# Kernel tuning notes

Measured on AMD Instinct MI355X. Metric: run time of the kernel, lower is better.

Reference implementation:

```python
import jax, jax.numpy as jnp
import numpy as np

I, H, O = 8, 32, 1  # input_size, hidden_size, output_size


def setup_inputs() -> dict:
    key = jax.random.key(0)
    ks = jax.random.split(key, 7)
    B, T = 4096, 256
    s_ih = 1.0 / np.sqrt(H)
    inp = {
        "x": jax.random.normal(ks[0], (B, T, I), dtype=jnp.float32),
        # PyTorch nn.LSTM params, gate order [i, f, g, o]
        "W_ih": jax.random.uniform(ks[1], (4 * H, I), minval=-s_ih, maxval=s_ih, dtype=jnp.float32),
        "W_hh": jax.random.uniform(ks[2], (4 * H, H), minval=-s_ih, maxval=s_ih, dtype=jnp.float32),
        "b_ih": jax.random.uniform(ks[3], (4 * H,), minval=-s_ih, maxval=s_ih, dtype=jnp.float32),
        "b_hh": jax.random.uniform(ks[4], (4 * H,), minval=-s_ih, maxval=s_ih, dtype=jnp.float32),
        # nn.Linear(H, O)
        "W_out": jax.random.uniform(ks[5], (O, H), minval=-s_ih, maxval=s_ih, dtype=jnp.float32),
        "b_out": jax.random.uniform(ks[6], (O,), minval=-s_ih, maxval=s_ih, dtype=jnp.float32),
    }
    return inp


def _lstm_last_h(x, W_ih, W_hh, b_ih, b_hh):
    B = x.shape[0]
    # Precompute input projections for all steps: [T, B, 4H]
    x_proj = jnp.einsum("bti,gi->tbg", x, W_ih) + (b_ih + b_hh)
    h0 = jnp.zeros((B, H), dtype=x.dtype)
    c0 = jnp.zeros((B, H), dtype=x.dtype)

    def step(carry, xp):
        h, c = carry
        z = xp + h @ W_hh.T  # [B, 4H]
        i = jax.nn.sigmoid(z[:, 0 * H:1 * H])
        f = jax.nn.sigmoid(z[:, 1 * H:2 * H])
        g = jnp.tanh(z[:, 2 * H:3 * H])
        o = jax.nn.sigmoid(z[:, 3 * H:4 * H])
        c = f * c + i * g
        h = o * jnp.tanh(c)
        return (h, c), None

    (hT, _), _ = jax.lax.scan(step, (h0, c0), x_proj)
    return hT  # equals out[:, -1, :] for unidirectional batch_first LSTM


def reference(x, W_ih, W_hh, b_ih, b_hh, W_out, b_out):
    hT = _lstm_last_h(x, W_ih, W_hh, b_ih, b_hh)
    return hT @ W_out.T + b_out  # [B, O]
```

## Files before the change

kernel.cpp:

```cpp
#include <hip/hip_runtime.h>


#define T_LEN   256
#define HALF_T  128
#define XSTRIDE 130
#define LOG2E   1.4426950408889634f

typedef short bf16x8 __attribute__((ext_vector_type(8)));
typedef float f32x4  __attribute__((ext_vector_type(4)));
typedef unsigned u32x4 __attribute__((ext_vector_type(4)));

static __device__ inline short f2bf_rne(float f) {
    union { float f; unsigned u; } v; v.f = f;
    unsigned u = v.u;
    return (short)((u + 0x7FFFu + ((u >> 16) & 1u)) >> 16);
}
static __device__ inline unsigned pack_bf2(float a, float b) {
    union { float f; unsigned u; } x, y; x.f = a; y.f = b;
    return ((x.u + 0x8000u) >> 16) | ((y.u + 0x8000u) & 0xFFFF0000u);
}
static __device__ inline float bf2f(short s) {
    union { unsigned u; float f; } v;
    v.u = ((unsigned)(unsigned short)s) << 16;
    return v.f;
}

__global__ __launch_bounds__(256) void lstm_kernel(
    const float* __restrict__ x, const float* __restrict__ W_ih,
    const float* __restrict__ W_hh, const float* __restrict__ b_ih,
    const float* __restrict__ b_hh, const float* __restrict__ W_out,
    const float* __restrict__ b_out, float* __restrict__ out)
{
    __shared__ __attribute__((aligned(16))) short xl[HALF_T * XSTRIDE];
    __shared__ __attribute__((aligned(16))) short h_lds[2][16 * 40];

    const int tid  = threadIdx.x;
    const int w    = tid >> 6;
    const int lane = tid & 63;
    const int L    = lane & 15;
    const int q    = lane >> 4;
    const int row0 = blockIdx.x * 16;
    const float4* xv = (const float4*)x;

    bf16x8 whh[2], wih[2];
    f32x4  bias[2];
#pragma unroll
    for (int e = 0; e < 2; ++e) {
        const int   n = 32 * (L & 3) + 8 * (L >> 2) + 2 * w + e;
        const float s = ((L & 3) == 2 ? 2.f * LOG2E : LOG2E);
        const float* src = W_hh + n * 32 + q * 8;
        bf16x8 fr;
#pragma unroll
        for (int j = 0; j < 8; ++j) fr[j] = f2bf_rne(src[j] * s);
        whh[e] = fr;
        bf16x8 gr = (bf16x8){0,0,0,0,0,0,0,0};
        if (q == 0) {
            const float* s2 = W_ih + n * 8;
#pragma unroll
            for (int j = 0; j < 8; ++j) gr[j] = f2bf_rne(s2[j] * s);
        }
        wih[e] = gr;
        f32x4 bb;
#pragma unroll
        for (int r = 0; r < 4; ++r) {
            const int   nr = 32 * r + 8 * q + 2 * w + e;
            const float sr = (r == 2 ? 2.f * LOG2E : LOG2E);
            bb[r] = (b_ih[nr] + b_hh[nr]) * sr;
        }
        bias[e] = bb;
    }

    for (int i = tid; i < 16 * 40; i += 256) h_lds[0][i] = 0;

#pragma unroll
    for (int it = 0; it < 8; ++it) {
        const int idx = tid + (it << 8);
        const int L2  = idx >> 7;
        const int tl  = idx & (HALF_T - 1);
        const float4* srcp = xv + ((size_t)(row0 + L2) * T_LEN + tl) * 2;
        const float4 a = srcp[0], b = srcp[1];
        u32x4 u;
        u[0] = pack_bf2(a.x, a.y); u[1] = pack_bf2(a.z, a.w);
        u[2] = pack_bf2(b.x, b.y); u[3] = pack_bf2(b.z, b.w);
        *(u32x4*)(&xl[tl * XSTRIDE + L2 * 8]) = u;
    }
    __syncthreads();

    f32x4 zx[2];
    {
        const bf16x8 xf0 = *(const bf16x8*)(&xl[L * 8]);
        zx[0] = __builtin_amdgcn_mfma_f32_16x16x32_bf16(wih[0], xf0, bias[0], 0, 0, 0);
        zx[1] = __builtin_amdgcn_mfma_f32_16x16x32_bf16(wih[1], xf0, bias[1], 0, 0, 0);
    }

    float c0 = 0.f, c1 = 0.f;

#pragma unroll 2
    for (int t = 0; t < T_LEN; ++t) {
        if (t == HALF_T - 1) {
#pragma unroll
            for (int it = 0; it < 8; ++it) {
                const int idx = tid + (it << 8);
                const int L2  = idx >> 7;
                const int tl  = idx & (HALF_T - 1);
                const float4* srcp = xv + ((size_t)(row0 + L2) * T_LEN + HALF_T + tl) * 2;
                const float4 a = srcp[0], b = srcp[1];
                u32x4 u;
                u[0] = pack_bf2(a.x, a.y); u[1] = pack_bf2(a.z, a.w);
                u[2] = pack_bf2(b.x, b.y); u[3] = pack_bf2(b.z, b.w);
                *(u32x4*)(&xl[tl * XSTRIDE + L2 * 8]) = u;
            }
            __syncthreads();
        }

        const int par = t & 1, nxt = par ^ 1;

        const bf16x8 hfrag = *(const bf16x8*)(&h_lds[par][L * 40 + q * 8]);
        int tn = t + 1; if (tn >= T_LEN) tn = T_LEN - 1;
        const bf16x8 xfrag = *(const bf16x8*)(&xl[(tn & (HALF_T - 1)) * XSTRIDE + L * 8]);

        const f32x4 a0 = __builtin_amdgcn_mfma_f32_16x16x32_bf16(whh[0], hfrag, zx[0], 0, 0, 0);
        const f32x4 a1 = __builtin_amdgcn_mfma_f32_16x16x32_bf16(whh[1], hfrag, zx[1], 0, 0, 0);
        zx[0] = __builtin_amdgcn_mfma_f32_16x16x32_bf16(wih[0], xfrag, bias[0], 0, 0, 0);
        zx[1] = __builtin_amdgcn_mfma_f32_16x16x32_bf16(wih[1], xfrag, bias[1], 0, 0, 0);

        float h0, h1;
        {
            const float ei = __builtin_amdgcn_exp2f(-a0[0]);
            const float ef = __builtin_amdgcn_exp2f(-a0[1]);
            const float eg = __builtin_amdgcn_exp2f(-a0[2]);
            const float eo = __builtin_amdgcn_exp2f(-a0[3]);
            const float fv = __builtin_amdgcn_rcpf(1.f + ef);
            const float ig = (1.f - eg) * __builtin_amdgcn_rcpf((1.f + ei) * (1.f + eg));
            c0 = fmaf(fv, c0, ig);
            const float ec = __builtin_amdgcn_exp2f(fminf(c0 * (-2.f * LOG2E), 40.f));
            h0 = (1.f - ec) * __builtin_amdgcn_rcpf((1.f + eo) * (1.f + ec));
        }
        {
            const float ei = __builtin_amdgcn_exp2f(-a1[0]);
            const float ef = __builtin_amdgcn_exp2f(-a1[1]);
            const float eg = __builtin_amdgcn_exp2f(-a1[2]);
            const float eo = __builtin_amdgcn_exp2f(-a1[3]);
            const float fv = __builtin_amdgcn_rcpf(1.f + ef);
            const float ig = (1.f - eg) * __builtin_amdgcn_rcpf((1.f + ei) * (1.f + eg));
            c1 = fmaf(fv, c1, ig);
            const float ec = __builtin_amdgcn_exp2f(fminf(c1 * (-2.f * LOG2E), 40.f));
            h1 = (1.f - ec) * __builtin_amdgcn_rcpf((1.f + eo) * (1.f + ec));
        }

        *(unsigned*)(&h_lds[nxt][L * 40 + 8 * q + 2 * w]) = pack_bf2(h0, h1);

        __syncthreads();
    }

    if (tid < 16) {
        float s = b_out[0];
#pragma unroll
        for (int k = 0; k < 32; ++k) s = fmaf(bf2f(h_lds[0][tid * 40 + k]), W_out[k], s);
        out[row0 + tid] = s;
    }
}

extern "C" void kernel_launch(void* const* d_in, const int* in_sizes, int n_in,
                              void* d_out, int out_size, void* d_ws, size_t ws_size,
                              hipStream_t stream) {
    const float* x     = (const float*)d_in[0];
    const float* W_ih  = (const float*)d_in[1];
    const float* W_hh  = (const float*)d_in[2];
    const float* b_ih  = (const float*)d_in[3];
    const float* b_hh  = (const float*)d_in[4];
    const float* W_out = (const float*)d_in[5];
    const float* b_out = (const float*)d_in[6];
    float* out = (float*)d_out;

    const int B = in_sizes[0] / (T_LEN * 8);
    const int tiles = B / 16;
    lstm_kernel<<<tiles, 256, 0, stream>>>(x, W_ih, W_hh, b_ih, b_hh, W_out, b_out, out);
}
```

Baseline: 147.8 us.

## Halve batch rows per block to double block count and occupancy

Each block now handles 8 batch rows instead of 16, launching twice as many blocks, with the x staging buffer halved and launch bounds requesting two blocks per CU. The MFMA N dimension still spans 16 columns, so rows are duplicated (L&7) and half the compute is redundant. The weight row mapping is permuted across waves, and the next-step input projection MFMA is moved after the h store to overlap with the barrier. The intent is more parallelism across CUs and latency hiding for the serial recurrence, at the cost of wasted MFMA work.

```diff
diff --git a/kernel.cpp b/kernel.cpp
--- a/kernel.cpp
+++ b/kernel.cpp
@@ -3,7 +3,7 @@
 
 #define T_LEN   256
 #define HALF_T  128
-#define XSTRIDE 130
+#define XSTRIDE 66
 #define LOG2E   1.4426950408889634f
 
 typedef short bf16x8 __attribute__((ext_vector_type(8)));
@@ -25,7 +25,7 @@
     return v.f;
 }
 
-__global__ __launch_bounds__(256) void lstm_kernel(
+__global__ __launch_bounds__(256, 2) void lstm_kernel(
     const float* __restrict__ x, const float* __restrict__ W_ih,
     const float* __restrict__ W_hh, const float* __restrict__ b_ih,
     const float* __restrict__ b_hh, const float* __restrict__ W_out,
@@ -39,31 +39,31 @@
     const int lane = tid & 63;
     const int L    = lane & 15;
     const int q    = lane >> 4;
-    const int row0 = blockIdx.x * 16;
+    const int rbase = blockIdx.x * 8;
     const float4* xv = (const float4*)x;
 
     bf16x8 whh[2], wih[2];
     f32x4  bias[2];
 #pragma unroll
     for (int e = 0; e < 2; ++e) {
-        const int   n = 32 * (L & 3) + 8 * (L >> 2) + 2 * w + e;
-        const float s = ((L & 3) == 2 ? 2.f * LOG2E : LOG2E);
+        const int   n  = 32 * (L & 3) + 8 * w + 2 * (L >> 2) + e;
+        const float sc = ((L & 3) == 2 ? 2.f * LOG2E : LOG2E);
         const float* src = W_hh + n * 32 + q * 8;
         bf16x8 fr;
 #pragma unroll
-        for (int j = 0; j < 8; ++j) fr[j] = f2bf_rne(src[j] * s);
+        for (int j = 0; j < 8; ++j) fr[j] = f2bf_rne(src[j] * sc);
         whh[e] = fr;
         bf16x8 gr = (bf16x8){0,0,0,0,0,0,0,0};
         if (q == 0) {
             const float* s2 = W_ih + n * 8;
 #pragma unroll
-            for (int j = 0; j < 8; ++j) gr[j] = f2bf_rne(s2[j] * s);
+            for (int j = 0; j < 8; ++j) gr[j] = f2bf_rne(s2[j] * sc);
         }
         wih[e] = gr;
         f32x4 bb;
 #pragma unroll
         for (int r = 0; r < 4; ++r) {
-            const int   nr = 32 * r + 8 * q + 2 * w + e;
+            const int   nr = 32 * r + 8 * w + 2 * q + e;
             const float sr = (r == 2 ? 2.f * LOG2E : LOG2E);
             bb[r] = (b_ih[nr] + b_hh[nr]) * sr;
         }
@@ -73,11 +73,11 @@
     for (int i = tid; i < 16 * 40; i += 256) h_lds[0][i] = 0;
 
 #pragma unroll
-    for (int it = 0; it < 8; ++it) {
+    for (int it = 0; it < 4; ++it) {
         const int idx = tid + (it << 8);
+        const int tl  = idx & (HALF_T - 1);
         const int L2  = idx >> 7;
-        const int tl  = idx & (HALF_T - 1);
-        const float4* srcp = xv + ((size_t)(row0 + L2) * T_LEN + tl) * 2;
+        const float4* srcp = xv + ((size_t)(rbase + L2) * T_LEN + tl) * 2;
         const float4 a = srcp[0], b = srcp[1];
         u32x4 u;
         u[0] = pack_bf2(a.x, a.y); u[1] = pack_bf2(a.z, a.w);
@@ -88,22 +88,23 @@
 
     f32x4 zx[2];
     {
-        const bf16x8 xf0 = *(const bf16x8*)(&xl[L * 8]);
+        const bf16x8 xf0 = *(const bf16x8*)(&xl[(L & 7) * 8]);
         zx[0] = __builtin_amdgcn_mfma_f32_16x16x32_bf16(wih[0], xf0, bias[0], 0, 0, 0);
         zx[1] = __builtin_amdgcn_mfma_f32_16x16x32_bf16(wih[1], xf0, bias[1], 0, 0, 0);
     }
 
     float c0 = 0.f, c1 = 0.f;
+    const int hwo = L * 40 + 8 * w + 2 * q;
 
 #pragma unroll 2
     for (int t = 0; t < T_LEN; ++t) {
         if (t == HALF_T - 1) {
 #pragma unroll
-            for (int it = 0; it < 8; ++it) {
+            for (int it = 0; it < 4; ++it) {
                 const int idx = tid + (it << 8);
+                const int tl  = idx & (HALF_T - 1);
                 const int L2  = idx >> 7;
-                const int tl  = idx & (HALF_T - 1);
-                const float4* srcp = xv + ((size_t)(row0 + L2) * T_LEN + HALF_T + tl) * 2;
+                const float4* srcp = xv + ((size_t)(rbase + L2) * T_LEN + HALF_T + tl) * 2;
                 const float4 a = srcp[0], b = srcp[1];
                 u32x4 u;
                 u[0] = pack_bf2(a.x, a.y); u[1] = pack_bf2(a.z, a.w);
@@ -116,13 +117,9 @@
         const int par = t & 1, nxt = par ^ 1;
 
         const bf16x8 hfrag = *(const bf16x8*)(&h_lds[par][L * 40 + q * 8]);
-        int tn = t + 1; if (tn >= T_LEN) tn = T_LEN - 1;
-        const bf16x8 xfrag = *(const bf16x8*)(&xl[(tn & (HALF_T - 1)) * XSTRIDE + L * 8]);
 
         const f32x4 a0 = __builtin_amdgcn_mfma_f32_16x16x32_bf16(whh[0], hfrag, zx[0], 0, 0, 0);
         const f32x4 a1 = __builtin_amdgcn_mfma_f32_16x16x32_bf16(whh[1], hfrag, zx[1], 0, 0, 0);
-        zx[0] = __builtin_amdgcn_mfma_f32_16x16x32_bf16(wih[0], xfrag, bias[0], 0, 0, 0);
-        zx[1] = __builtin_amdgcn_mfma_f32_16x16x32_bf16(wih[1], xfrag, bias[1], 0, 0, 0);
 
         float h0, h1;
         {
@@ -148,16 +145,23 @@
             h1 = (1.f - ec) * __builtin_amdgcn_rcpf((1.f + eo) * (1.f + ec));
         }
 
-        *(unsigned*)(&h_lds[nxt][L * 40 + 8 * q + 2 * w]) = pack_bf2(h0, h1);
+        *(unsigned*)(&h_lds[nxt][hwo]) = pack_bf2(h0, h1);
+
+        {
+            int tn = t + 1; if (tn >= T_LEN) tn = T_LEN - 1;
+            const bf16x8 xfrag = *(const bf16x8*)(&xl[(tn & (HALF_T - 1)) * XSTRIDE + (L & 7) * 8]);
+            zx[0] = __builtin_amdgcn_mfma_f32_16x16x32_bf16(wih[0], xfrag, bias[0], 0, 0, 0);
+            zx[1] = __builtin_amdgcn_mfma_f32_16x16x32_bf16(wih[1], xfrag, bias[1], 0, 0, 0);
+        }
 
         __syncthreads();
     }
 
-    if (tid < 16) {
+    if (tid < 8) {
         float s = b_out[0];
 #pragma unroll
         for (int k = 0; k < 32; ++k) s = fmaf(bf2f(h_lds[0][tid * 40 + k]), W_out[k], s);
-        out[row0 + tid] = s;
+        out[rbase + tid] = s;
     }
 }
 
@@ -174,6 +178,6 @@
     float* out = (float*)d_out;
 
     const int B = in_sizes[0] / (T_LEN * 8);
-    const int tiles = B / 16;
-    lstm_kernel<<<tiles, 256, 0, stream>>>(x, W_ih, W_hh, b_ih, b_hh, W_out, b_out, out);
+    const int blocks = B / 8;
+    lstm_kernel<<<blocks, 256, 0, stream>>>(x, W_ih, W_hh, b_ih, b_hh, W_out, b_out, out);
 }
```

Measured after the change: 168.3 us. 13.9% more time.

## Interleave two 16-row batch tiles per block to overlap recurrent latency

Applied to the files above, without the earlier changes.

Each block now processes 32 batch rows as two independent 16-row recurrences, issuing their MFMAs and gate math interleaved so one tile's latency hides the other's. Input staging switches to 64-step chunks reloaded four times instead of two halves. This halves the grid to 128 blocks, leaving many CUs idle, in exchange for more instruction-level parallelism per step and fewer barriers per row.

```diff
diff --git a/kernel.cpp b/kernel.cpp
--- a/kernel.cpp
+++ b/kernel.cpp
@@ -2,7 +2,7 @@
 
 
 #define T_LEN   256
-#define HALF_T  128
+#define CH      64
 #define XSTRIDE 130
 #define LOG2E   1.4426950408889634f
 
@@ -31,33 +31,33 @@
     const float* __restrict__ b_hh, const float* __restrict__ W_out,
     const float* __restrict__ b_out, float* __restrict__ out)
 {
-    __shared__ __attribute__((aligned(16))) short xl[HALF_T * XSTRIDE];
-    __shared__ __attribute__((aligned(16))) short h_lds[2][16 * 40];
+    __shared__ __attribute__((aligned(16))) short xl[2][CH * XSTRIDE];
+    __shared__ __attribute__((aligned(16))) short h_lds[2][2][16 * 40];
 
     const int tid  = threadIdx.x;
     const int w    = tid >> 6;
     const int lane = tid & 63;
     const int L    = lane & 15;
     const int q    = lane >> 4;
-    const int row0 = blockIdx.x * 16;
+    const int rbase = blockIdx.x * 32;
     const float4* xv = (const float4*)x;
 
     bf16x8 whh[2], wih[2];
     f32x4  bias[2];
 #pragma unroll
     for (int e = 0; e < 2; ++e) {
-        const int   n = 32 * (L & 3) + 8 * (L >> 2) + 2 * w + e;
-        const float s = ((L & 3) == 2 ? 2.f * LOG2E : LOG2E);
+        const int   n  = 32 * (L & 3) + 8 * (L >> 2) + 2 * w + e;
+        const float sc = ((L & 3) == 2 ? 2.f * LOG2E : LOG2E);
         const float* src = W_hh + n * 32 + q * 8;
         bf16x8 fr;
 #pragma unroll
-        for (int j = 0; j < 8; ++j) fr[j] = f2bf_rne(src[j] * s);
+        for (int j = 0; j < 8; ++j) fr[j] = f2bf_rne(src[j] * sc);
         whh[e] = fr;
         bf16x8 gr = (bf16x8){0,0,0,0,0,0,0,0};
         if (q == 0) {
             const float* s2 = W_ih + n * 8;
 #pragma unroll
-            for (int j = 0; j < 8; ++j) gr[j] = f2bf_rne(s2[j] * s);
+            for (int j = 0; j < 8; ++j) gr[j] = f2bf_rne(s2[j] * sc);
         }
         wih[e] = gr;
         f32x4 bb;
@@ -70,94 +70,107 @@
         bias[e] = bb;
     }
 
-    for (int i = tid; i < 16 * 40; i += 256) h_lds[0][i] = 0;
+    for (int i = tid; i < 2 * 2 * 16 * 40; i += 256) ((short*)h_lds)[i] = 0;
 
 #pragma unroll
     for (int it = 0; it < 8; ++it) {
         const int idx = tid + (it << 8);
-        const int L2  = idx >> 7;
-        const int tl  = idx & (HALF_T - 1);
-        const float4* srcp = xv + ((size_t)(row0 + L2) * T_LEN + tl) * 2;
+        const int tau = idx >> 10;
+        const int rem = idx & 1023;
+        const int tl  = rem & (CH - 1);
+        const int L2  = rem >> 6;
+        const float4* srcp = xv + ((size_t)(rbase + tau * 16 + L2) * T_LEN + tl) * 2;
         const float4 a = srcp[0], b = srcp[1];
         u32x4 u;
         u[0] = pack_bf2(a.x, a.y); u[1] = pack_bf2(a.z, a.w);
         u[2] = pack_bf2(b.x, b.y); u[3] = pack_bf2(b.z, b.w);
-        *(u32x4*)(&xl[tl * XSTRIDE + L2 * 8]) = u;
+        *(u32x4*)(&xl[tau][tl * XSTRIDE + L2 * 8]) = u;
     }
     __syncthreads();
 
-    f32x4 zx[2];
-    {
-        const bf16x8 xf0 = *(const bf16x8*)(&xl[L * 8]);
-        zx[0] = __builtin_amdgcn_mfma_f32_16x16x32_bf16(wih[0], xf0, bias[0], 0, 0, 0);
-        zx[1] = __builtin_amdgcn_mfma_f32_16x16x32_bf16(wih[1], xf0, bias[1], 0, 0, 0);
+    f32x4 zx[2][2];
+#pragma unroll
+    for (int tau = 0; tau < 2; ++tau) {
+        const bf16x8 xf0 = *(const bf16x8*)(&xl[tau][L * 8]);
+        zx[tau][0] = __builtin_amdgcn_mfma_f32_16x16x32_bf16(wih[0], xf0, bias[0], 0, 0, 0);
+        zx[tau][1] = __builtin_amdgcn_mfma_f32_16x16x32_bf16(wih[1], xf0, bias[1], 0, 0, 0);
     }
 
-    float c0 = 0.f, c1 = 0.f;
+    float c[2][2] = {{0.f, 0.f}, {0.f, 0.f}};
+    const int hwo = L * 40 + 8 * q + 2 * w;
+    const int hro = L * 40 + q * 8;
 
 #pragma unroll 2
     for (int t = 0; t < T_LEN; ++t) {
-        if (t == HALF_T - 1) {
+        if ((t & (CH - 1)) == CH - 1 && t != T_LEN - 1) {
+            const int ck = (t >> 6) + 1;
 #pragma unroll
             for (int it = 0; it < 8; ++it) {
                 const int idx = tid + (it << 8);
-                const int L2  = idx >> 7;
-                const int tl  = idx & (HALF_T - 1);
-                const float4* srcp = xv + ((size_t)(row0 + L2) * T_LEN + HALF_T + tl) * 2;
+                const int tau = idx >> 10;
+                const int rem = idx & 1023;
+                const int tl  = rem & (CH - 1);
+                const int L2  = rem >> 6;
+                const float4* srcp = xv + ((size_t)(rbase + tau * 16 + L2) * T_LEN + CH * ck + tl) * 2;
                 const float4 a = srcp[0], b = srcp[1];
                 u32x4 u;
                 u[0] = pack_bf2(a.x, a.y); u[1] = pack_bf2(a.z, a.w);
                 u[2] = pack_bf2(b.x, b.y); u[3] = pack_bf2(b.z, b.w);
-                *(u32x4*)(&xl[tl * XSTRIDE + L2 * 8]) = u;
+                *(u32x4*)(&xl[tau][tl * XSTRIDE + L2 * 8]) = u;
             }
             __syncthreads();
         }
 
         const int par = t & 1, nxt = par ^ 1;
 
-        const bf16x8 hfrag = *(const bf16x8*)(&h_lds[par][L * 40 + q * 8]);
-        int tn = t + 1; if (tn >= T_LEN) tn = T_LEN - 1;
-        const bf16x8 xfrag = *(const bf16x8*)(&xl[(tn & (HALF_T - 1)) * XSTRIDE + L * 8]);
+        const bf16x8 hfA = *(const bf16x8*)(&h_lds[0][par][hro]);
+        const bf16x8 hfB = *(const bf16x8*)(&h_lds[1][par][hro]);
 
-        const f32x4 a0 = __builtin_amdgcn_mfma_f32_16x16x32_bf16(whh[0], hfrag, zx[0], 0, 0, 0);
-        const f32x4 a1 = __builtin_amdgcn_mfma_f32_16x16x32_bf16(whh[1], hfrag, zx[1], 0, 0, 0);
-        zx[0] = __builtin_amdgcn_mfma_f32_16x16x32_bf16(wih[0], xfrag, bias[0], 0, 0, 0);
-        zx[1] = __builtin_amdgcn_mfma_f32_16x16x32_bf16(wih[1], xfrag, bias[1], 0, 0, 0);
+        const f32x4 aA0 = __builtin_amdgcn_mfma_f32_16x16x32_bf16(whh[0], hfA, zx[0][0], 0, 0, 0);
+        const f32x4 aB0 = __builtin_amdgcn_mfma_f32_16x16x32_bf16(whh[0], hfB, zx[1][0], 0, 0, 0);
+        const f32x4 aA1 = __builtin_amdgcn_mfma_f32_16x16x32_bf16(whh[1], hfA, zx[0][1], 0, 0, 0);
+        const f32x4 aB1 = __builtin_amdgcn_mfma_f32_16x16x32_bf16(whh[1], hfB, zx[1][1], 0, 0, 0);
 
-        float h0, h1;
-        {
-            const float ei = __builtin_amdgcn_exp2f(-a0[0]);
-            const float ef = __builtin_amdgcn_exp2f(-a0[1]);
-            const float eg = __builtin_amdgcn_exp2f(-a0[2]);
-            const float eo = __builtin_amdgcn_exp2f(-a0[3]);
-            const float fv = __builtin_amdgcn_rcpf(1.f + ef);
-            const float ig = (1.f - eg) * __builtin_amdgcn_rcpf((1.f + ei) * (1.f + eg));
-            c0 = fmaf(fv, c0, ig);
-            const float ec = __builtin_amdgcn_exp2f(fminf(c0 * (-2.f * LOG2E), 40.f));
-            h0 = (1.f - ec) * __builtin_amdgcn_rcpf((1.f + eo) * (1.f + ec));
-        }
-        {
-            const float ei = __builtin_amdgcn_exp2f(-a1[0]);
-            const float ef = __builtin_amdgcn_exp2f(-a1[1]);
-            const float eg = __builtin_amdgcn_exp2f(-a1[2]);
-            const float eo = __builtin_amdgcn_exp2f(-a1[3]);
-            const float fv = __builtin_amdgcn_rcpf(1.f + ef);
-            const float ig = (1.f - eg) * __builtin_amdgcn_rcpf((1.f + ei) * (1.f + eg));
-            c1 = fmaf(fv, c1, ig);
-            const float ec = __builtin_amdgcn_exp2f(fminf(c1 * (-2.f * LOG2E), 40.f));
-            h1 = (1.f - ec) * __builtin_amdgcn_rcpf((1.f + eo) * (1.f + ec));
+        const f32x4 accs[2][2] = {{aA0, aA1}, {aB0, aB1}};
+#pragma unroll
+        for (int tau = 0; tau < 2; ++tau) {
+            float hv[2];
+#pragma unroll
+            for (int e = 0; e < 2; ++e) {
+                const f32x4 a = accs[tau][e];
+                const float ei = __builtin_amdgcn_exp2f(-a[0]);
+                const float ef = __builtin_amdgcn_exp2f(-a[1]);
+                const float eg = __builtin_amdgcn_exp2f(-a[2]);
+                const float eo = __builtin_amdgcn_exp2f(-a[3]);
+                const float fv = __builtin_amdgcn_rcpf(1.f + ef);
+                const float ig = (1.f - eg) * __builtin_amdgcn_rcpf((1.f + ei) * (1.f + eg));
+                c[tau][e] = fmaf(fv, c[tau][e], ig);
+                const float ec = __builtin_amdgcn_exp2f(fminf(c[tau][e] * (-2.f * LOG2E), 40.f));
+                hv[e] = (1.f - ec) * __builtin_amdgcn_rcpf((1.f + eo) * (1.f + ec));
+            }
+            *(unsigned*)(&h_lds[tau][nxt][hwo]) = pack_bf2(hv[0], hv[1]);
         }
 
-        *(unsigned*)(&h_lds[nxt][L * 40 + 8 * q + 2 * w]) = pack_bf2(h0, h1);
+        {
+            int tn = t + 1; if (tn >= T_LEN) tn = T_LEN - 1;
+            const int xo = (tn & (CH - 1)) * XSTRIDE + L * 8;
+            const bf16x8 xfA = *(const bf16x8*)(&xl[0][xo]);
+            const bf16x8 xfB = *(const bf16x8*)(&xl[1][xo]);
+            zx[0][0] = __builtin_amdgcn_mfma_f32_16x16x32_bf16(wih[0], xfA, bias[0], 0, 0, 0);
+            zx[0][1] = __builtin_amdgcn_mfma_f32_16x16x32_bf16(wih[1], xfA, bias[1], 0, 0, 0);
+            zx[1][0] = __builtin_amdgcn_mfma_f32_16x16x32_bf16(wih[0], xfB, bias[0], 0, 0, 0);
+            zx[1][1] = __builtin_amdgcn_mfma_f32_16x16x32_bf16(wih[1], xfB, bias[1], 0, 0, 0);
+        }
 
         __syncthreads();
     }
 
-    if (tid < 16) {
+    if (tid < 32) {
+        const int tau = tid >> 4, r = tid & 15;
         float s = b_out[0];
 #pragma unroll
-        for (int k = 0; k < 32; ++k) s = fmaf(bf2f(h_lds[0][tid * 40 + k]), W_out[k], s);
-        out[row0 + tid] = s;
+        for (int k = 0; k < 32; ++k) s = fmaf(bf2f(h_lds[tau][0][r * 40 + k]), W_out[k], s);
+        out[rbase + tau * 16 + r] = s;
     }
 }
 
@@ -174,6 +187,6 @@
     float* out = (float*)d_out;
 
     const int B = in_sizes[0] / (T_LEN * 8);
-    const int tiles = B / 16;
-    lstm_kernel<<<tiles, 256, 0, stream>>>(x, W_ih, W_hh, b_ih, b_hh, W_out, b_out, out);
+    const int blocks = B / 32;
+    lstm_kernel<<<blocks, 256, 0, stream>>>(x, W_ih, W_hh, b_ih, b_hh, W_out, b_out, out);
 }
```

Result: slower. 206.9 us (+40.0%).
